# Kernel tuning notes

Hardware: AMD Instinct MI355X
Metric: run time of the kernel (lower is better)

## Reference

```python
import jax, jax.numpy as jnp
import numpy as np

D_MODEL = 1024
NUM_HEADS = 16
D_K = D_MODEL // NUM_HEADS


def setup_inputs() -> dict:
    key = jax.random.key(0)
    ks = jax.random.split(key, 11)
    B, S = 2, 2048
    scale = 1.0 / np.sqrt(D_MODEL)
    inp = {
        "Q_in": jax.random.normal(ks[0], (B, S, D_MODEL), jnp.float32),
        "K_in": jax.random.normal(ks[1], (B, S, D_MODEL), jnp.float32),
        "V_in": jax.random.normal(ks[2], (B, S, D_MODEL), jnp.float32),
        "Wq": jax.random.normal(ks[3], (D_MODEL, D_MODEL), jnp.float32) * scale,
        "bq": jnp.zeros((D_MODEL,), jnp.float32),
        "Wk": jax.random.normal(ks[4], (D_MODEL, D_MODEL), jnp.float32) * scale,
        "bk": jnp.zeros((D_MODEL,), jnp.float32),
        "Wv": jax.random.normal(ks[5], (D_MODEL, D_MODEL), jnp.float32) * scale,
        "bv": jnp.zeros((D_MODEL,), jnp.float32),
        "Wfc": jax.random.normal(ks[6], (D_MODEL, D_MODEL), jnp.float32) * scale,
        "bfc": jnp.zeros((D_MODEL,), jnp.float32),
    }
    return inp


def _split_heads(x, B):
    # [B, S, D] -> [B, H, S, d_k]
    return x.reshape(B, -1, NUM_HEADS, D_K).transpose(0, 2, 1, 3)


def reference(Q_in, K_in, V_in, Wq, bq, Wk, bk, Wv, bv, Wfc, bfc):
    B = Q_in.shape[0]
    q = _split_heads(Q_in @ Wq + bq, B)
    k = _split_heads(K_in @ Wk + bk, B)
    v = _split_heads(V_in @ Wv + bv, B)
    # scaled dot-product attention (mask=None)
    scores = jnp.einsum("bhqd,bhkd->bhqk", q, k) / jnp.sqrt(jnp.float32(D_K))
    attn = jax.nn.softmax(scores, axis=-1)
    ctx = jnp.einsum("bhqk,bhkd->bhqd", attn, v)
    out = ctx.transpose(0, 2, 1, 3).reshape(B, -1, D_MODEL)
    out = out @ Wfc + bfc
    return out, attn
```

## Files before the change

kernel.cpp:

```cpp
#include <hip/hip_runtime.h>

typedef unsigned short u16;
typedef _Float16 f16;
typedef __attribute__((ext_vector_type(8))) f16 f16x8;
typedef __attribute__((ext_vector_type(4))) float f32x4;
typedef __attribute__((ext_vector_type(4))) u16 u16x4;
typedef __attribute__((ext_vector_type(8))) u16 u16x8;

__device__ __forceinline__ u16 f2h(float x){
  f16 h = (f16)x;
  return __builtin_bit_cast(u16, h);
}

__device__ __forceinline__ void stage16(const void* g, void* l){
  __builtin_amdgcn_global_load_lds(
      (const __attribute__((address_space(1))) unsigned*)g,
      (__attribute__((address_space(3))) unsigned*)l, 16, 0, 0);
}

__global__ __launch_bounds__(256) void convert_x3(
    const float* __restrict__ in0, const float* __restrict__ in1, const float* __restrict__ in2,
    u16* __restrict__ o0, u16* __restrict__ o1, u16* __restrict__ o2){
  const int b = blockIdx.x >> 12;
  const int i = (blockIdx.x & 4095) * 256 + threadIdx.x;
  const float* in = (b == 0) ? in0 : (b == 1) ? in1 : in2;
  u16* out = (b == 0) ? o0 : (b == 1) ? o1 : o2;
  f32x4 v = ((const f32x4*)in)[i];
  u16x4 h;
  #pragma unroll
  for (int j = 0; j < 4; j++) h[j] = f2h(v[j]);
  ((u16x4*)out)[i] = h;
}

__global__ __launch_bounds__(256) void transpose_w4(
    const float* __restrict__ W0, const float* __restrict__ W1,
    const float* __restrict__ W2, const float* __restrict__ W3,
    u16* __restrict__ t0, u16* __restrict__ t1, u16* __restrict__ t2, u16* __restrict__ t3){
  __shared__ float tile[64][68];
  const int z = blockIdx.z;
  const float* W = (z == 0) ? W0 : (z == 1) ? W1 : (z == 2) ? W2 : W3;
  u16* wt = (z == 0) ? t0 : (z == 1) ? t1 : (z == 2) ? t2 : t3;
  const int tid = threadIdx.x;
  const int k0 = blockIdx.y * 64, n0 = blockIdx.x * 64;
  #pragma unroll
  for (int g = 0; g < 4; g++){
    int flat4 = g * 256 + tid;
    int row = flat4 >> 4, c4 = flat4 & 15;
    f32x4 v = *(const f32x4*)&W[(size_t)(k0 + row) * 1024 + n0 + c4 * 4];
    *(f32x4*)&tile[row][c4 * 4] = v;
  }
  __syncthreads();
  const int n = tid >> 2, kc = (tid & 3) * 16;
  u16x8 o0, o1;
  #pragma unroll
  for (int j = 0; j < 8; j++){
    o0[j] = f2h(tile[kc + j][n]);
    o1[j] = f2h(tile[kc + 8 + j][n]);
  }
  u16* dst = &wt[(size_t)(n0 + n) * 1024 + k0 + kc];
  *(u16x8*)dst = o0;
  *(u16x8*)(dst + 8) = o1;
}

template<int MODE>
__device__ __forceinline__ void gemm_body(
    const u16* __restrict__ A, const u16* __restrict__ B,
    const float* __restrict__ bias,
    float* __restrict__ outF, u16* __restrict__ outH,
    int N, int K, int bx, int by)
{
  __shared__ u16 sA[128 * 32];
  __shared__ u16 sB[128 * 32];
  const int tid = threadIdx.x;
  const int wid = tid >> 6, lane = tid & 63;
  const int lm = lane & 15, lg = lane >> 4;
  const int bm = by * 128, bn = bx * 128;
  const int wrow = (wid >> 1) * 64, wcol = (wid & 1) * 64;
  const int srow = tid >> 2;
  const int skc  = (tid & 3) * 8;

  f32x4 acc[4][4] = {};

  for (int kt = 0; kt < K; kt += 32){
    {
      char* dA = (char*)sA + wid * 1024;
      char* dB = (char*)sB + wid * 1024;
      stage16(A + (size_t)(bm +      srow) * K + kt + skc, dA);
      stage16(A + (size_t)(bm + 64 + srow) * K + kt + skc, dA + 4096);
      stage16(B + (size_t)(bn +      srow) * K + kt + skc, dB);
      stage16(B + (size_t)(bn + 64 + srow) * K + kt + skc, dB + 4096);
    }
    __syncthreads();
    f16x8 af[4], bf[4];
    #pragma unroll
    for (int mf = 0; mf < 4; mf++)
      af[mf] = *(const f16x8*)&sA[(wrow + mf * 16 + lm) * 32 + lg * 8];
    #pragma unroll
    for (int nf = 0; nf < 4; nf++)
      bf[nf] = *(const f16x8*)&sB[(wcol + nf * 16 + lm) * 32 + lg * 8];
    #pragma unroll
    for (int mf = 0; mf < 4; mf++)
      #pragma unroll
      for (int nf = 0; nf < 4; nf++)
        acc[mf][nf] = __builtin_amdgcn_mfma_f32_16x16x32_f16(af[mf], bf[nf], acc[mf][nf], 0, 0, 0);
    __syncthreads();
  }

  #pragma unroll
  for (int mf = 0; mf < 4; mf++)
    #pragma unroll
    for (int nf = 0; nf < 4; nf++){
      const int n  = bn + wcol + nf * 16 + lm;
      const int mb = bm + wrow + mf * 16 + lg * 4;
      #pragma unroll
      for (int r = 0; r < 4; r++){
        const int m = mb + r;
        float v = acc[mf][nf][r] + ((MODE == 2) ? bias[m] : bias[n]);
        if constexpr (MODE == 0){
          outF[(size_t)m * N + n] = v;
        } else if constexpr (MODE == 1){
          const size_t idx = (((size_t)((m >> 11) * 16 + (n >> 6))) * 2048 + (m & 2047)) * 64 + (n & 63);
          outH[idx] = f2h(v);
        } else {
          const size_t idx = (((size_t)((n >> 11) * 16 + (m >> 6))) * 64 + (m & 63)) * 2048 + (n & 2047);
          outH[idx] = f2h(v);
        }
      }
    }
}

__global__ __launch_bounds__(256, 2) void gemm_qk(
    const u16* __restrict__ xq, const u16* __restrict__ wqt, const float* __restrict__ bq, u16* __restrict__ qh,
    const u16* __restrict__ xk, const u16* __restrict__ wkt, const float* __restrict__ bk, u16* __restrict__ kh){
  const int z = blockIdx.z;
  const u16* A = z ? xk : xq;
  const u16* B = z ? wkt : wqt;
  const float* bias = z ? bk : bq;
  u16* out = z ? kh : qh;
  gemm_body<1>(A, B, bias, nullptr, out, 1024, 1024, blockIdx.x, blockIdx.y);
}

__global__ __launch_bounds__(256, 2) void gemm_v(
    const u16* __restrict__ wvt, const u16* __restrict__ xv, const float* __restrict__ bv, u16* __restrict__ vt){
  gemm_body<2>(wvt, xv, bv, nullptr, vt, 4096, 1024, blockIdx.x, blockIdx.y);
}

__global__ __launch_bounds__(256, 2) void gemm_fc(
    const u16* __restrict__ ctx, const u16* __restrict__ wft, const float* __restrict__ bfc, float* __restrict__ outF){
  gemm_body<0>(ctx, wft, bfc, outF, nullptr, 1024, 1024, blockIdx.x, blockIdx.y);
}

__global__ __launch_bounds__(256, 4) void attn_fused(
    const u16* __restrict__ qh_, const u16* __restrict__ kh_,
    const u16* __restrict__ vt_,
    float* __restrict__ attn_out, u16* __restrict__ ctx)
{
  constexpr int S = 2048;
  __shared__ __align__(16) u16 te[4][16][40];
  const int tid = threadIdx.x, wid = tid >> 6, lane = tid & 63;
  const int lm = lane & 15, lg = lane >> 4;
  const int wg = blockIdx.x;
  const int xcd = wg & 7, li = wg >> 3;
  const int bh = (xcd << 2) + (li >> 5);
  const int q0 = (li & 31) * 64 + wid * 16;
  const size_t base = (size_t)bh * S * 64;
  const u16* Qh = qh_ + base;
  const u16* Kh = kh_ + base;
  const u16* Vt = vt_ + base;
  float* Aout = attn_out + (size_t)bh * S * S;

  f16x8 qb[2];
  #pragma unroll
  for (int ks = 0; ks < 2; ks++)
    qb[ks] = *(const f16x8*)(Qh + (size_t)(q0 + lm) * 64 + ks * 32 + lg * 8);

  const float SCL2 = 0.18033688011112042f;

  float part = 0.0f;
  for (int nt = 0; nt < 128; nt += 2){
    const u16* kp0 = Kh + (size_t)(nt * 16 + lm) * 64 + lg * 8;
    const u16* kp1 = kp0 + 16 * 64;
    f16x8 k00 = *(const f16x8*)(kp0);
    f16x8 k01 = *(const f16x8*)(kp0 + 32);
    f16x8 k10 = *(const f16x8*)(kp1);
    f16x8 k11 = *(const f16x8*)(kp1 + 32);
    f32x4 c0 = {}, c1 = {};
    c0 = __builtin_amdgcn_mfma_f32_16x16x32_f16(k00, qb[0], c0, 0, 0, 0);
    c0 = __builtin_amdgcn_mfma_f32_16x16x32_f16(k01, qb[1], c0, 0, 0, 0);
    c1 = __builtin_amdgcn_mfma_f32_16x16x32_f16(k10, qb[0], c1, 0, 0, 0);
    c1 = __builtin_amdgcn_mfma_f32_16x16x32_f16(k11, qb[1], c1, 0, 0, 0);
    #pragma unroll
    for (int r = 0; r < 4; r++){
      part += __builtin_amdgcn_exp2f(c0[r] * SCL2);
      part += __builtin_amdgcn_exp2f(c1[r] * SCL2);
    }
  }
  part += __shfl_xor(part, 16);
  part += __shfl_xor(part, 32);
  const float inv = 1.0f / part;

  f32x4 cacc[4] = {};
  for (int nt2 = 0; nt2 < 64; nt2++){
    f16x8 vb[4];
    #pragma unroll
    for (int nf = 0; nf < 4; nf++)
      vb[nf] = *(const f16x8*)(Vt + (size_t)(nf * 16 + lm) * S + nt2 * 32 + lg * 8);

    const u16* kp0 = Kh + (size_t)(nt2 * 32 + lm) * 64 + lg * 8;
    const u16* kp1 = kp0 + 16 * 64;
    f16x8 k00 = *(const f16x8*)(kp0);
    f16x8 k01 = *(const f16x8*)(kp0 + 32);
    f16x8 k10 = *(const f16x8*)(kp1);
    f16x8 k11 = *(const f16x8*)(kp1 + 32);
    f32x4 c0 = {}, c1 = {};
    c0 = __builtin_amdgcn_mfma_f32_16x16x32_f16(k00, qb[0], c0, 0, 0, 0);
    c0 = __builtin_amdgcn_mfma_f32_16x16x32_f16(k01, qb[1], c0, 0, 0, 0);
    c1 = __builtin_amdgcn_mfma_f32_16x16x32_f16(k10, qb[0], c1, 0, 0, 0);
    c1 = __builtin_amdgcn_mfma_f32_16x16x32_f16(k11, qb[1], c1, 0, 0, 0);

    #pragma unroll
    for (int half = 0; half < 2; half++){
      f32x4 c = half ? c1 : c0;
      float a[4];
      #pragma unroll
      for (int r = 0; r < 4; r++)
        a[r] = __builtin_amdgcn_exp2f(c[r] * SCL2) * inv;
      f32x4 av = { a[0], a[1], a[2], a[3] };
      float* dst = Aout + (size_t)(q0 + lm) * S + (nt2 * 2 + half) * 16 + lg * 4;
      __builtin_nontemporal_store(av, (f32x4*)dst);
      u16x4 hp;
      #pragma unroll
      for (int r = 0; r < 4; r++) hp[r] = f2h(a[r]);
      *(u16x4*)&te[wid][lm][half * 16 + lg * 4] = hp;
    }
    f16x8 pa = *(const f16x8*)&te[wid][lm][lg * 8];
    #pragma unroll
    for (int nf = 0; nf < 4; nf++)
      cacc[nf] = __builtin_amdgcn_mfma_f32_16x16x32_f16(pa, vb[nf], cacc[nf], 0, 0, 0);
  }

  const int b = bh >> 4, h = bh & 15;
  #pragma unroll
  for (int nf = 0; nf < 4; nf++)
    #pragma unroll
    for (int r = 0; r < 4; r++){
      int srow2 = q0 + lg * 4 + r;
      int d = nf * 16 + lm;
      ctx[(size_t)(b * 2048 + srow2) * 1024 + h * 64 + d] = f2h(cacc[nf][r]);
    }
}

extern "C" void kernel_launch(void* const* d_in, const int* in_sizes, int n_in,
                              void* d_out, int out_size, void* d_ws, size_t ws_size,
                              hipStream_t stream) {
  const float* Qi  = (const float*)d_in[0];
  const float* Ki  = (const float*)d_in[1];
  const float* Vi  = (const float*)d_in[2];
  const float* Wq  = (const float*)d_in[3];
  const float* bq  = (const float*)d_in[4];
  const float* Wk  = (const float*)d_in[5];
  const float* bk  = (const float*)d_in[6];
  const float* Wv  = (const float*)d_in[7];
  const float* bv  = (const float*)d_in[8];
  const float* Wfc = (const float*)d_in[9];
  const float* bfc = (const float*)d_in[10];

  char* w = (char*)d_ws;
  const size_t P  = 8388608;
  const size_t PW = 2097152;
  u16* xq  = (u16*)(w + 0*P);
  u16* xk  = (u16*)(w + 1*P);
  u16* xv  = (u16*)(w + 2*P);
  u16* qh  = (u16*)(w + 3*P);
  u16* kh  = (u16*)(w + 4*P);
  u16* vt  = (u16*)(w + 5*P);
  u16* ctx = (u16*)(w + 6*P);
  char* w2 = w + 7*P;
  u16* wqt = (u16*)(w2 + 0*PW);
  u16* wkt = (u16*)(w2 + 1*PW);
  u16* wvt = (u16*)(w2 + 2*PW);
  u16* wft = (u16*)(w2 + 3*PW);

  float* outp  = (float*)d_out;
  float* attnp = outp + 4194304;

  convert_x3<<<12288, 256, 0, stream>>>(Qi, Ki, Vi, xq, xk, xv);
  transpose_w4<<<dim3(16, 16, 4), 256, 0, stream>>>(Wq, Wk, Wv, Wfc, wqt, wkt, wvt, wft);

  gemm_qk<<<dim3(8, 32, 2), 256, 0, stream>>>(xq, wqt, bq, qh, xk, wkt, bk, kh);
  gemm_v<<<dim3(32, 8), 256, 0, stream>>>(wvt, xv, bv, vt);
  attn_fused<<<1024, 256, 0, stream>>>(qh, kh, vt, attnp, ctx);
  gemm_fc<<<dim3(8, 32), 256, 0, stream>>>(ctx, wft, bfc, outp);
}
```

Before: 456.6 us.

## Split attention keys across waves and coalesce attention-probability stores

Each block now handles 16 query rows, with the four waves splitting the 2048 keys into 512-key slices. Row sums and context partials are reduced across waves through shared memory, and the grid grows to 4096 blocks. Attention probabilities are staged through LDS and written as contiguous 32-column row segments instead of scattered 16-byte pieces. In exchange, the stored fp32 attention values now pass through fp16 rounding, and the kernel adds extra syncs and LDS traffic.

Measured after the change: 452.4 us. No clear change (-0.9%).

```diff
diff --git a/kernel.cpp b/kernel.cpp
--- a/kernel.cpp
+++ b/kernel.cpp
@@ -10,6 +10,9 @@
 __device__ __forceinline__ u16 f2h(float x){
   f16 h = (f16)x;
   return __builtin_bit_cast(u16, h);
+}
+__device__ __forceinline__ float h2f(u16 v){
+  return (float)__builtin_bit_cast(f16, v);
 }
 
 __device__ __forceinline__ void stage16(const void* g, void* l){
@@ -133,11 +136,8 @@
     const u16* __restrict__ xq, const u16* __restrict__ wqt, const float* __restrict__ bq, u16* __restrict__ qh,
     const u16* __restrict__ xk, const u16* __restrict__ wkt, const float* __restrict__ bk, u16* __restrict__ kh){
   const int z = blockIdx.z;
-  const u16* A = z ? xk : xq;
-  const u16* B = z ? wkt : wqt;
-  const float* bias = z ? bk : bq;
-  u16* out = z ? kh : qh;
-  gemm_body<1>(A, B, bias, nullptr, out, 1024, 1024, blockIdx.x, blockIdx.y);
+  gemm_body<1>(z ? xk : xq, z ? wkt : wqt, z ? bk : bq, nullptr, z ? kh : qh,
+               1024, 1024, blockIdx.x, blockIdx.y);
 }
 
 __global__ __launch_bounds__(256, 2) void gemm_v(
@@ -157,17 +157,20 @@
 {
   constexpr int S = 2048;
   __shared__ __align__(16) u16 te[4][16][40];
+  __shared__ float sred[4][16];
+  __shared__ __align__(16) float cred[4][64][20];
   const int tid = threadIdx.x, wid = tid >> 6, lane = tid & 63;
   const int lm = lane & 15, lg = lane >> 4;
   const int wg = blockIdx.x;
   const int xcd = wg & 7, li = wg >> 3;
-  const int bh = (xcd << 2) + (li >> 5);
-  const int q0 = (li & 31) * 64 + wid * 16;
+  const int bh = (xcd << 2) + (li >> 7);
+  const int q0 = (li & 127) * 16;
   const size_t base = (size_t)bh * S * 64;
   const u16* Qh = qh_ + base;
   const u16* Kh = kh_ + base;
   const u16* Vt = vt_ + base;
   float* Aout = attn_out + (size_t)bh * S * S;
+  const int kbase = wid * 512;
 
   f16x8 qb[2];
   #pragma unroll
@@ -176,9 +179,9 @@
 
   const float SCL2 = 0.18033688011112042f;
 
-  float part = 0.0f;
-  for (int nt = 0; nt < 128; nt += 2){
-    const u16* kp0 = Kh + (size_t)(nt * 16 + lm) * 64 + lg * 8;
+  float part0 = 0.0f, part1 = 0.0f;
+  for (int nt2 = 0; nt2 < 16; nt2++){
+    const u16* kp0 = Kh + (size_t)(kbase + nt2 * 32 + lm) * 64 + lg * 8;
     const u16* kp1 = kp0 + 16 * 64;
     f16x8 k00 = *(const f16x8*)(kp0);
     f16x8 k01 = *(const f16x8*)(kp0 + 32);
@@ -191,22 +194,28 @@
     c1 = __builtin_amdgcn_mfma_f32_16x16x32_f16(k11, qb[1], c1, 0, 0, 0);
     #pragma unroll
     for (int r = 0; r < 4; r++){
-      part += __builtin_amdgcn_exp2f(c0[r] * SCL2);
-      part += __builtin_amdgcn_exp2f(c1[r] * SCL2);
-    }
-  }
+      part0 += __builtin_amdgcn_exp2f(c0[r] * SCL2);
+      part1 += __builtin_amdgcn_exp2f(c1[r] * SCL2);
+    }
+  }
+  float part = part0 + part1;
   part += __shfl_xor(part, 16);
   part += __shfl_xor(part, 32);
-  const float inv = 1.0f / part;
-
+  if (lane < 16) sred[wid][lm] = part;
+  __syncthreads();
+  const float inv = 1.0f / (sred[0][lm] + sred[1][lm] + sred[2][lm] + sred[3][lm]);
+
+  const int sq = lane >> 3;
+  const int sc = (lane & 7) * 4;
   f32x4 cacc[4] = {};
-  for (int nt2 = 0; nt2 < 64; nt2++){
+  for (int nt2 = 0; nt2 < 16; nt2++){
+    const int col0 = kbase + nt2 * 32;
     f16x8 vb[4];
     #pragma unroll
     for (int nf = 0; nf < 4; nf++)
-      vb[nf] = *(const f16x8*)(Vt + (size_t)(nf * 16 + lm) * S + nt2 * 32 + lg * 8);
-
-    const u16* kp0 = Kh + (size_t)(nt2 * 32 + lm) * 64 + lg * 8;
+      vb[nf] = *(const f16x8*)(Vt + (size_t)(nf * 16 + lm) * S + col0 + lg * 8);
+
+    const u16* kp0 = Kh + (size_t)(col0 + lm) * 64 + lg * 8;
     const u16* kp1 = kp0 + 16 * 64;
     f16x8 k00 = *(const f16x8*)(kp0);
     f16x8 k01 = *(const f16x8*)(kp0 + 32);
@@ -221,33 +230,41 @@
     #pragma unroll
     for (int half = 0; half < 2; half++){
       f32x4 c = half ? c1 : c0;
-      float a[4];
+      u16x4 hp;
       #pragma unroll
       for (int r = 0; r < 4; r++)
-        a[r] = __builtin_amdgcn_exp2f(c[r] * SCL2) * inv;
-      f32x4 av = { a[0], a[1], a[2], a[3] };
-      float* dst = Aout + (size_t)(q0 + lm) * S + (nt2 * 2 + half) * 16 + lg * 4;
-      __builtin_nontemporal_store(av, (f32x4*)dst);
-      u16x4 hp;
-      #pragma unroll
-      for (int r = 0; r < 4; r++) hp[r] = f2h(a[r]);
+        hp[r] = f2h(__builtin_amdgcn_exp2f(c[r] * SCL2) * inv);
       *(u16x4*)&te[wid][lm][half * 16 + lg * 4] = hp;
     }
     f16x8 pa = *(const f16x8*)&te[wid][lm][lg * 8];
     #pragma unroll
     for (int nf = 0; nf < 4; nf++)
       cacc[nf] = __builtin_amdgcn_mfma_f32_16x16x32_f16(pa, vb[nf], cacc[nf], 0, 0, 0);
-  }
-
+    #pragma unroll
+    for (int i2 = 0; i2 < 2; i2++){
+      const int q = i2 * 8 + sq;
+      u16x4 hv = *(const u16x4*)&te[wid][q][sc];
+      f32x4 av = { h2f(hv[0]), h2f(hv[1]), h2f(hv[2]), h2f(hv[3]) };
+      __builtin_nontemporal_store(av, (f32x4*)(Aout + (size_t)(q0 + q) * S + col0 + sc));
+    }
+  }
+
+  #pragma unroll
+  for (int nf = 0; nf < 4; nf++)
+    *(f32x4*)&cred[wid][nf * 16 + lm][lg * 4] = cacc[nf];
+  __syncthreads();
   const int b = bh >> 4, h = bh & 15;
-  #pragma unroll
-  for (int nf = 0; nf < 4; nf++)
-    #pragma unroll
-    for (int r = 0; r < 4; r++){
-      int srow2 = q0 + lg * 4 + r;
-      int d = nf * 16 + lm;
-      ctx[(size_t)(b * 2048 + srow2) * 1024 + h * 64 + d] = f2h(cacc[nf][r]);
-    }
+  const int rd = lane;
+  const int rq = wid * 4;
+  f32x4 s0 = *(const f32x4*)&cred[0][rd][rq];
+  f32x4 s1 = *(const f32x4*)&cred[1][rd][rq];
+  f32x4 s2 = *(const f32x4*)&cred[2][rd][rq];
+  f32x4 s3 = *(const f32x4*)&cred[3][rd][rq];
+  #pragma unroll
+  for (int j = 0; j < 4; j++){
+    float v = s0[j] + s1[j] + s2[j] + s3[j];
+    ctx[(size_t)(b * 2048 + q0 + rq + j) * 1024 + h * 64 + rd] = f2h(v);
+  }
 }
 
 extern "C" void kernel_launch(void* const* d_in, const int* in_sizes, int n_in,
@@ -289,6 +306,6 @@
 
   gemm_qk<<<dim3(8, 32, 2), 256, 0, stream>>>(xq, wqt, bq, qh, xk, wkt, bk, kh);
   gemm_v<<<dim3(32, 8), 256, 0, stream>>>(wvt, xv, bv, vt);
-  attn_fused<<<1024, 256, 0, stream>>>(qh, kh, vt, attnp, ctx);
+  attn_fused<<<4096, 256, 0, stream>>>(qh, kh, vt, attnp, ctx);
   gemm_fc<<<dim3(8, 32), 256, 0, stream>>>(ctx, wft, bfc, outp);
 }
```
